# Kernel optimization log

Hardware: AMD Instinct MI355X
Metric: run time of the kernel (lower is better)

Reference implementation:

```python
import jax, jax.numpy as jnp
import numpy as np


def setup_inputs() -> dict:
    key = jax.random.key(0)
    image = jax.random.randint(key, (4, 2048, 2048), 0, 50000, dtype=jnp.int32)
    return {"image": image}


def reference(image) -> jnp.ndarray:
    # Faithful, single-pass equivalent of LabelGapAdjustment(shift=False).
    # The original while-loop (decrement labels above each missing label until
    # labels are the consecutive set 1..K) is exactly dense-rank remapping:
    # new_label = 1-based rank of the label among the sorted unique labels.
    imin = image.min()
    image_shift = 1 - imin
    shifted = jnp.where(imin <= 0, image + image_shift, image)

    flat = shifted.reshape(-1)
    order = jnp.argsort(flat)
    s = flat[order]  # sorted labels
    # 1 where a new distinct value starts; cumsum -> 1-based dense rank
    is_new = jnp.concatenate(
        [jnp.ones((1,), dtype=jnp.int32), (s[1:] != s[:-1]).astype(jnp.int32)]
    )
    ranks_sorted = jnp.cumsum(is_new)  # [N], values 1..K
    # scatter ranks back to original positions
    ranks = jnp.zeros_like(flat).at[order].set(ranks_sorted.astype(flat.dtype))
    compact = ranks.reshape(image.shape)

    # shift=False: undo the shift (original subtracts image_shift unconditionally)
    return compact - image_shift
```

## Files before the change

kernel.cpp:

```cpp
#include <hip/hip_runtime.h>
#include <limits.h>

#define TABLE 65536
#define NBITW (TABLE / 32)
#define NTAB  512
#define CHUNK 16
#define NCHUNK (NTAB / CHUNK)
#define MIN_OFF 0
#define PACK_OFF 64
#define PART_OFF (PACK_OFF + 2 * NBITW)
#define TAB_OFF  (PART_OFF + NCHUNK * NBITW)

typedef int ivec4 __attribute__((ext_vector_type(4)));

__global__ __launch_bounds__(1024) void lga_mark_kernel(const int* __restrict__ img,
                                                        int n, int n4, int* ws) {
    __shared__ unsigned char tbl[TABLE];
    unsigned int* tbl32 = (unsigned int*)tbl;
    int t = threadIdx.x;
    for (int i = t; i < TABLE / 4; i += 1024) tbl32[i] = 0;
    __syncthreads();

    int stride = gridDim.x * blockDim.x;
    for (int i = blockIdx.x * blockDim.x + t; i < n4; i += stride) {
        ivec4 v = ((const ivec4*)img)[i];
        tbl[v.x] = 1;
        tbl[v.y] = 1;
        tbl[v.z] = 1;
        tbl[v.w] = 1;
    }
    if (blockIdx.x == 0 && t == 0) {
        for (int j = n4 * 4; j < n; ++j) tbl[img[j]] = 1;
    }
    __syncthreads();

    if (t < NBITW / 4) {
        uint4* mytab = (uint4*)((unsigned int*)(ws + TAB_OFF) + blockIdx.x * NBITW);
        unsigned int m[4];
        #pragma unroll
        for (int q = 0; q < 4; ++q) {
            const unsigned int* p = tbl32 + (4 * t + q) * 8;
            unsigned int mm = 0;
            #pragma unroll
            for (int j = 0; j < 8; ++j) {
                unsigned int w = p[j];
                mm |= (w & 1u) << (j * 4);
                mm |= ((w >> 8) & 1u) << (j * 4 + 1);
                mm |= ((w >> 16) & 1u) << (j * 4 + 2);
                mm |= ((w >> 24) & 1u) << (j * 4 + 3);
            }
            m[q] = mm;
        }
        mytab[t] = make_uint4(m[0], m[1], m[2], m[3]);
    }
}

__global__ __launch_bounds__(128) void lga_merge_kernel(int* ws) {
    int d4 = blockIdx.x * 128 + threadIdx.x;
    const uint4* tabs = (const uint4*)((const unsigned int*)(ws + TAB_OFF)
                                       + (size_t)blockIdx.y * CHUNK * NBITW);
    unsigned int m0 = 0, m1 = 0, m2 = 0, m3 = 0;
    #pragma unroll
    for (int k = 0; k < CHUNK; ++k) {
        uint4 v = tabs[k * (NBITW / 4) + d4];
        m0 |= v.x; m1 |= v.y; m2 |= v.z; m3 |= v.w;
    }
    uint4* part = (uint4*)((unsigned int*)(ws + PART_OFF) + (size_t)blockIdx.y * NBITW);
    part[d4] = make_uint4(m0, m1, m2, m3);
}

__global__ __launch_bounds__(1024) void lga_scan_kernel(int* ws) {
    const unsigned int* part = (const unsigned int*)(ws + PART_OFF);
    uint4* pack = (uint4*)(ws + PACK_OFF);
    int t = threadIdx.x;
    int lane = t & 63;
    int wave = t >> 6;

    unsigned int d0 = 0, d1 = 0;
    #pragma unroll
    for (int c = 0; c < NCHUNK; ++c) {
        d0 |= part[c * NBITW + 2 * t];
        d1 |= part[c * NBITW + 2 * t + 1];
    }
    int c0 = __popc(d0);
    int s = c0 + __popc(d1);
    int firstset;
    if (d0)      firstset = 64 * t + __ffs(d0) - 1;
    else if (d1) firstset = 64 * t + 32 + __ffs(d1) - 1;
    else         firstset = INT_MAX;

    int v = s;
    #pragma unroll
    for (int off = 1; off < 64; off <<= 1) {
        int u = __shfl_up(v, off, 64);
        if (lane >= off) v += u;
    }
    int fm = firstset;
    #pragma unroll
    for (int off = 32; off > 0; off >>= 1)
        fm = min(fm, __shfl_down(fm, off, 64));

    __shared__ int wsum[16];
    __shared__ int wmin[16];
    if (lane == 63) wsum[wave] = v;
    if (lane == 0)  wmin[wave] = fm;
    __syncthreads();
    if (wave == 0 && lane < 16) {
        int w = wsum[lane];
        #pragma unroll
        for (int off = 1; off < 16; off <<= 1) {
            int u = __shfl_up(w, off, 16);
            if (lane >= off) w += u;
        }
        wsum[lane] = w;
        int m = wmin[lane];
        #pragma unroll
        for (int off = 8; off > 0; off >>= 1)
            m = min(m, __shfl_down(m, off, 16));
        if (lane == 0) ws[MIN_OFF] = m;
    }
    __syncthreads();

    unsigned int excl = (unsigned int)(v - s + (wave > 0 ? wsum[wave - 1] : 0));
    pack[t] = make_uint4(excl, d0, excl + (unsigned int)c0, d1);
}

__global__ __launch_bounds__(1024) void lga_remap_kernel(const int* __restrict__ img,
                                                         int* __restrict__ out,
                                                         int n, int n4,
                                                         const int* __restrict__ ws) {
    __shared__ uint2 lp[NBITW];
    const uint2* pack = (const uint2*)(ws + PACK_OFF);
    int t = threadIdx.x;
    for (int i = t; i < NBITW; i += 1024) lp[i] = pack[i];
    int imin = ws[MIN_OFF];
    __syncthreads();

    int tid = blockIdx.x * blockDim.x + t;
    int stride = gridDim.x * blockDim.x;

    #define RANK1(vv) ({ uint2 _p = lp[((unsigned)(vv)) >> 5]; \
                         (int)(_p.x + __popc(_p.y & ((1u << ((vv) & 31)) - 1u))) + imin; })

    int i = tid;
    for (; i + stride < n4; i += 2 * stride) {
        ivec4 va = ((const ivec4*)img)[i];
        ivec4 vb = ((const ivec4*)img)[i + stride];
        ivec4 ra, rb;
        ra.x = RANK1(va.x); ra.y = RANK1(va.y); ra.z = RANK1(va.z); ra.w = RANK1(va.w);
        rb.x = RANK1(vb.x); rb.y = RANK1(vb.y); rb.z = RANK1(vb.z); rb.w = RANK1(vb.w);
        __builtin_nontemporal_store(ra, (ivec4*)out + i);
        __builtin_nontemporal_store(rb, (ivec4*)out + i + stride);
    }
    if (i < n4) {
        ivec4 va = ((const ivec4*)img)[i];
        ivec4 ra;
        ra.x = RANK1(va.x); ra.y = RANK1(va.y); ra.z = RANK1(va.z); ra.w = RANK1(va.w);
        __builtin_nontemporal_store(ra, (ivec4*)out + i);
    }
    if (blockIdx.x == 0 && t == 0) {
        for (int j = n4 * 4; j < n; ++j) {
            int vv = img[j];
            out[j] = RANK1(vv);
        }
    }
    #undef RANK1
}

extern "C" void kernel_launch(void* const* d_in, const int* in_sizes, int n_in,
                              void* d_out, int out_size, void* d_ws, size_t ws_size,
                              hipStream_t stream) {
    const int* img = (const int*)d_in[0];
    int* out = (int*)d_out;
    int* ws = (int*)d_ws;
    int n = in_sizes[0];
    int n4 = n / 4;

    lga_mark_kernel<<<NTAB, 1024, 0, stream>>>(img, n, n4, ws);
    lga_merge_kernel<<<dim3(NBITW / 512, NCHUNK), 128, 0, stream>>>(ws);
    lga_scan_kernel<<<1, 1024, 0, stream>>>(ws);
    lga_remap_kernel<<<512, 1024, 0, stream>>>(img, out, n, n4, ws);
}
```

Baseline: 128.8 us.

## Fuse mark/merge/scan/remap into one cooperative kernel holding image in registers

Replaces four separate launches with a single cooperative-groups kernel of 256 blocks that uses grid.sync between the mark, merge, scan and remap phases. Each thread loads its 16 vec4 image elements once into registers and reuses them for both marking and remapping, so the second read of the 64 MB image is avoided. The cost is three grid-wide barriers, a single-block scan phase while the rest of the grid waits, and high register pressure from holding 64 ints per thread. If the cooperative launch fails, the code falls back to the four-kernel path with 256 mark blocks.

```diff
diff --git a/kernel.cpp b/kernel.cpp
--- a/kernel.cpp
+++ b/kernel.cpp
@@ -1,11 +1,16 @@
 #include <hip/hip_runtime.h>
+#include <hip/hip_cooperative_groups.h>
 #include <limits.h>
+
+namespace cg = cooperative_groups;
 
 #define TABLE 65536
 #define NBITW (TABLE / 32)
-#define NTAB  512
+#define NBLK  256
+#define NTHR  1024
+#define PAYLOAD 16
 #define CHUNK 16
-#define NCHUNK (NTAB / CHUNK)
+#define NCHUNK (NBLK / CHUNK)
 #define MIN_OFF 0
 #define PACK_OFF 64
 #define PART_OFF (PACK_OFF + 2 * NBITW)
@@ -13,66 +18,29 @@
 
 typedef int ivec4 __attribute__((ext_vector_type(4)));
 
-__global__ __launch_bounds__(1024) void lga_mark_kernel(const int* __restrict__ img,
-                                                        int n, int n4, int* ws) {
-    __shared__ unsigned char tbl[TABLE];
-    unsigned int* tbl32 = (unsigned int*)tbl;
-    int t = threadIdx.x;
-    for (int i = t; i < TABLE / 4; i += 1024) tbl32[i] = 0;
-    __syncthreads();
-
-    int stride = gridDim.x * blockDim.x;
-    for (int i = blockIdx.x * blockDim.x + t; i < n4; i += stride) {
-        ivec4 v = ((const ivec4*)img)[i];
-        tbl[v.x] = 1;
-        tbl[v.y] = 1;
-        tbl[v.z] = 1;
-        tbl[v.w] = 1;
-    }
-    if (blockIdx.x == 0 && t == 0) {
-        for (int j = n4 * 4; j < n; ++j) tbl[img[j]] = 1;
-    }
-    __syncthreads();
-
-    if (t < NBITW / 4) {
-        uint4* mytab = (uint4*)((unsigned int*)(ws + TAB_OFF) + blockIdx.x * NBITW);
-        unsigned int m[4];
+__device__ __forceinline__ void flush_tbl_to_bits(const unsigned int* tbl32, int t,
+                                                  unsigned int* mytab_dw) {
+    unsigned int m[2];
+    #pragma unroll
+    for (int q = 0; q < 2; ++q) {
+        const unsigned int* p = tbl32 + (2 * t + q) * 8;
+        unsigned int mm = 0;
         #pragma unroll
-        for (int q = 0; q < 4; ++q) {
-            const unsigned int* p = tbl32 + (4 * t + q) * 8;
-            unsigned int mm = 0;
-            #pragma unroll
-            for (int j = 0; j < 8; ++j) {
-                unsigned int w = p[j];
-                mm |= (w & 1u) << (j * 4);
-                mm |= ((w >> 8) & 1u) << (j * 4 + 1);
-                mm |= ((w >> 16) & 1u) << (j * 4 + 2);
-                mm |= ((w >> 24) & 1u) << (j * 4 + 3);
-            }
-            m[q] = mm;
-        }
-        mytab[t] = make_uint4(m[0], m[1], m[2], m[3]);
-    }
-}
-
-__global__ __launch_bounds__(128) void lga_merge_kernel(int* ws) {
-    int d4 = blockIdx.x * 128 + threadIdx.x;
-    const uint4* tabs = (const uint4*)((const unsigned int*)(ws + TAB_OFF)
-                                       + (size_t)blockIdx.y * CHUNK * NBITW);
-    unsigned int m0 = 0, m1 = 0, m2 = 0, m3 = 0;
-    #pragma unroll
-    for (int k = 0; k < CHUNK; ++k) {
-        uint4 v = tabs[k * (NBITW / 4) + d4];
-        m0 |= v.x; m1 |= v.y; m2 |= v.z; m3 |= v.w;
-    }
-    uint4* part = (uint4*)((unsigned int*)(ws + PART_OFF) + (size_t)blockIdx.y * NBITW);
-    part[d4] = make_uint4(m0, m1, m2, m3);
-}
-
-__global__ __launch_bounds__(1024) void lga_scan_kernel(int* ws) {
+        for (int j = 0; j < 8; ++j) {
+            unsigned int w = p[j];
+            mm |= (w & 1u) << (j * 4);
+            mm |= ((w >> 8) & 1u) << (j * 4 + 1);
+            mm |= ((w >> 16) & 1u) << (j * 4 + 2);
+            mm |= ((w >> 24) & 1u) << (j * 4 + 3);
+        }
+        m[q] = mm;
+    }
+    ((uint2*)mytab_dw)[t] = make_uint2(m[0], m[1]);
+}
+
+__device__ __forceinline__ void scan_body(int* ws, int t, int* wsum, int* wmin) {
     const unsigned int* part = (const unsigned int*)(ws + PART_OFF);
     uint4* pack = (uint4*)(ws + PACK_OFF);
-    int t = threadIdx.x;
     int lane = t & 63;
     int wave = t >> 6;
 
@@ -100,8 +68,6 @@
     for (int off = 32; off > 0; off >>= 1)
         fm = min(fm, __shfl_down(fm, off, 64));
 
-    __shared__ int wsum[16];
-    __shared__ int wmin[16];
     if (lane == 63) wsum[wave] = v;
     if (lane == 0)  wmin[wave] = fm;
     __syncthreads();
@@ -123,6 +89,128 @@
 
     unsigned int excl = (unsigned int)(v - s + (wave > 0 ? wsum[wave - 1] : 0));
     pack[t] = make_uint4(excl, d0, excl + (unsigned int)c0, d1);
+}
+
+#define RANK1(lp, vx, imin) ({ uint2 _p = (lp)[((unsigned)(vx)) >> 5]; \
+    (int)(_p.x + __popc(_p.y & ((1u << ((vx) & 31)) - 1u))) + (imin); })
+
+__global__ __launch_bounds__(NTHR, 4) void lga_fused_kernel(
+        const int* __restrict__ img, int* __restrict__ out,
+        int n, int n4, int* __restrict__ ws) {
+    cg::grid_group grid = cg::this_grid();
+
+    __shared__ __align__(16) unsigned char smem[TABLE];
+    __shared__ int wsum[16], wmin[16];
+    unsigned int* tbl32 = (unsigned int*)smem;
+    int t = threadIdx.x;
+    int b = blockIdx.x;
+
+    for (int i = t; i < TABLE / 4; i += NTHR) tbl32[i] = 0;
+    __syncthreads();
+
+    const int base = b * NTHR + t;
+    const int STRIDE = NBLK * NTHR;
+    ivec4 v[PAYLOAD];
+    #pragma unroll
+    for (int k = 0; k < PAYLOAD; ++k) {
+        int idx = base + k * STRIDE;
+        if (idx < n4) v[k] = ((const ivec4*)img)[idx];
+    }
+    #pragma unroll
+    for (int k = 0; k < PAYLOAD; ++k) {
+        int idx = base + k * STRIDE;
+        if (idx < n4) {
+            smem[v[k].x] = 1;
+            smem[v[k].y] = 1;
+            smem[v[k].z] = 1;
+            smem[v[k].w] = 1;
+        }
+    }
+    if (b == 0 && t == 0) {
+        for (int j = n4 * 4; j < n; ++j) smem[img[j]] = 1;
+    }
+    __syncthreads();
+    flush_tbl_to_bits(tbl32, t, (unsigned int*)(ws + TAB_OFF) + b * NBITW);
+    grid.sync();
+
+    {
+        int chunk = b >> 4, slice = b & 15;
+        if (t < 128) {
+            int d = slice * 128 + t;
+            const unsigned int* tabs = (const unsigned int*)(ws + TAB_OFF)
+                                     + (size_t)chunk * CHUNK * NBITW;
+            unsigned int m = 0;
+            #pragma unroll
+            for (int k = 0; k < CHUNK; ++k) m |= tabs[k * NBITW + d];
+            ((unsigned int*)(ws + PART_OFF))[chunk * NBITW + d] = m;
+        }
+    }
+    grid.sync();
+
+    if (b == 0) scan_body(ws, t, wsum, wmin);
+    grid.sync();
+
+    uint2* lp = (uint2*)smem;
+    {
+        const uint2* pack = (const uint2*)(ws + PACK_OFF);
+        for (int i = t; i < NBITW; i += NTHR) lp[i] = pack[i];
+    }
+    int imin = ws[MIN_OFF];
+    __syncthreads();
+
+    #pragma unroll
+    for (int k = 0; k < PAYLOAD; ++k) {
+        int idx = base + k * STRIDE;
+        if (idx < n4) {
+            ivec4 r;
+            r.x = RANK1(lp, v[k].x, imin);
+            r.y = RANK1(lp, v[k].y, imin);
+            r.z = RANK1(lp, v[k].z, imin);
+            r.w = RANK1(lp, v[k].w, imin);
+            __builtin_nontemporal_store(r, (ivec4*)out + idx);
+        }
+    }
+    if (b == 0 && t == 0) {
+        for (int j = n4 * 4; j < n; ++j) {
+            int vx = img[j];
+            out[j] = RANK1(lp, vx, imin);
+        }
+    }
+}
+
+__global__ __launch_bounds__(1024) void lga_mark_kernel(const int* __restrict__ img,
+                                                        int n, int n4, int* ws) {
+    __shared__ __align__(16) unsigned char tbl[TABLE];
+    unsigned int* tbl32 = (unsigned int*)tbl;
+    int t = threadIdx.x;
+    for (int i = t; i < TABLE / 4; i += 1024) tbl32[i] = 0;
+    __syncthreads();
+
+    int stride = gridDim.x * blockDim.x;
+    for (int i = blockIdx.x * blockDim.x + t; i < n4; i += stride) {
+        ivec4 v = ((const ivec4*)img)[i];
+        tbl[v.x] = 1; tbl[v.y] = 1; tbl[v.z] = 1; tbl[v.w] = 1;
+    }
+    if (blockIdx.x == 0 && t == 0) {
+        for (int j = n4 * 4; j < n; ++j) tbl[img[j]] = 1;
+    }
+    __syncthreads();
+    flush_tbl_to_bits(tbl32, t, (unsigned int*)(ws + TAB_OFF) + blockIdx.x * NBITW);
+}
+
+__global__ __launch_bounds__(128) void lga_merge_kernel(int* ws) {
+    int d = blockIdx.x * 128 + threadIdx.x;
+    const unsigned int* tabs = (const unsigned int*)(ws + TAB_OFF)
+                             + (size_t)blockIdx.y * CHUNK * NBITW;
+    unsigned int m = 0;
+    #pragma unroll
+    for (int k = 0; k < CHUNK; ++k) m |= tabs[k * NBITW + d];
+    ((unsigned int*)(ws + PART_OFF))[blockIdx.y * NBITW + d] = m;
+}
+
+__global__ __launch_bounds__(1024) void lga_scan_kernel(int* ws) {
+    __shared__ int wsum[16], wmin[16];
+    scan_body(ws, threadIdx.x, wsum, wmin);
 }
 
 __global__ __launch_bounds__(1024) void lga_remap_kernel(const int* __restrict__ img,
@@ -136,35 +224,22 @@
     int imin = ws[MIN_OFF];
     __syncthreads();
 
-    int tid = blockIdx.x * blockDim.x + t;
     int stride = gridDim.x * blockDim.x;
-
-    #define RANK1(vv) ({ uint2 _p = lp[((unsigned)(vv)) >> 5]; \
-                         (int)(_p.x + __popc(_p.y & ((1u << ((vv) & 31)) - 1u))) + imin; })
-
-    int i = tid;
-    for (; i + stride < n4; i += 2 * stride) {
-        ivec4 va = ((const ivec4*)img)[i];
-        ivec4 vb = ((const ivec4*)img)[i + stride];
-        ivec4 ra, rb;
-        ra.x = RANK1(va.x); ra.y = RANK1(va.y); ra.z = RANK1(va.z); ra.w = RANK1(va.w);
-        rb.x = RANK1(vb.x); rb.y = RANK1(vb.y); rb.z = RANK1(vb.z); rb.w = RANK1(vb.w);
-        __builtin_nontemporal_store(ra, (ivec4*)out + i);
-        __builtin_nontemporal_store(rb, (ivec4*)out + i + stride);
-    }
-    if (i < n4) {
+    for (int i = blockIdx.x * blockDim.x + t; i < n4; i += stride) {
         ivec4 va = ((const ivec4*)img)[i];
         ivec4 ra;
-        ra.x = RANK1(va.x); ra.y = RANK1(va.y); ra.z = RANK1(va.z); ra.w = RANK1(va.w);
+        ra.x = RANK1(lp, va.x, imin);
+        ra.y = RANK1(lp, va.y, imin);
+        ra.z = RANK1(lp, va.z, imin);
+        ra.w = RANK1(lp, va.w, imin);
         __builtin_nontemporal_store(ra, (ivec4*)out + i);
     }
     if (blockIdx.x == 0 && t == 0) {
         for (int j = n4 * 4; j < n; ++j) {
-            int vv = img[j];
-            out[j] = RANK1(vv);
-        }
-    }
-    #undef RANK1
+            int vx = img[j];
+            out[j] = RANK1(lp, vx, imin);
+        }
+    }
 }
 
 extern "C" void kernel_launch(void* const* d_in, const int* in_sizes, int n_in,
@@ -176,8 +251,13 @@
     int n = in_sizes[0];
     int n4 = n / 4;
 
-    lga_mark_kernel<<<NTAB, 1024, 0, stream>>>(img, n, n4, ws);
-    lga_merge_kernel<<<dim3(NBITW / 512, NCHUNK), 128, 0, stream>>>(ws);
-    lga_scan_kernel<<<1, 1024, 0, stream>>>(ws);
-    lga_remap_kernel<<<512, 1024, 0, stream>>>(img, out, n, n4, ws);
-}
+    void* args[] = { (void*)&img, (void*)&out, (void*)&n, (void*)&n4, (void*)&ws };
+    hipError_t err = hipLaunchCooperativeKernel((const void*)lga_fused_kernel,
+                                                dim3(NBLK), dim3(NTHR), args, 0, stream);
+    if (err != hipSuccess) {
+        lga_mark_kernel<<<NBLK, NTHR, 0, stream>>>(img, n, n4, ws);
+        lga_merge_kernel<<<dim3(16, NCHUNK), 128, 0, stream>>>(ws);
+        lga_scan_kernel<<<1, 1024, 0, stream>>>(ws);
+        lga_remap_kernel<<<512, 1024, 0, stream>>>(img, out, n, n4, ws);
+    }
+}
```

New measurement: 216.9 us. +68.4%, slower.
